# Kernel tuning notes

Measured on AMD Instinct MI355X. Metric: run time of the kernel, lower is better.

Reference implementation:

```python
import jax, jax.numpy as jnp
import numpy as np

OUTPUT_DIM = 4096
INPUT_DIM = 2048
BATCH = 8192
SPARSITY = 0.02
BOOST_STRENGTH = 100.0
TOP_K = int(np.ceil(SPARSITY * OUTPUT_DIM))  # 82


def setup_inputs() -> dict:
    key = jax.random.key(0)
    k1, k2, k3, k4 = jax.random.split(key, 4)
    # Binary input activity pattern, as expected by an HTM spatial pooler.
    x = (jax.random.uniform(k1, (BATCH, INPUT_DIM)) < 0.3).astype(jnp.float32)
    # connection = round(uniform permanence) * bernoulli(pool_density=0.9) mask -> binary.
    perm = jnp.round(jax.random.uniform(k2, (INPUT_DIM, OUTPUT_DIM)))
    mask = (jax.random.uniform(k3, (INPUT_DIM, OUTPUT_DIM)) < 0.9).astype(jnp.float32)
    connection = perm * mask
    # Average duty-cycle activations are near the target sparsity (~0.02);
    # keeping them small also keeps exp(-boost_strength * diff) in fp32 range.
    avg_activation = jax.random.uniform(k4, (1, OUTPUT_DIM)) * 0.02
    return {"x": x, "connection": connection, "avg_activation": avg_activation}


def reference(x, connection, avg_activation) -> jnp.ndarray:
    D = connection.shape[1]
    # neighbor_activity = avg_activation @ (1 - I) / (D - 1)
    # == (sum(avg) - avg) / (D - 1), avoiding the dense [D, D] matmul.
    total = jnp.sum(avg_activation, axis=1, keepdims=True)  # [1, 1]
    neighbor_activity = (total - avg_activation) / (D - 1)  # [1, D]
    boost_factor = jnp.exp(-BOOST_STRENGTH * (avg_activation - neighbor_activity))
    overlap = jnp.matmul(x, connection) * boost_factor  # [B, D]
    _, act_idx = jax.lax.top_k(overlap, TOP_K)  # [B, TOP_K]
    batch_ids = jnp.arange(x.shape[0])[:, None]  # [B, 1]
    # Scatter 1.0 into a dense one-hot activation map.
    output = jnp.zeros_like(overlap).at[batch_ids, act_idx].set(1.0)
    return output
```

## Files before the change

### kernel.cpp

```cpp
#include <hip/hip_runtime.h>
#include <math.h>

#define M_DIM 8192
#define K_DIM 2048
#define N_DIM 4096
#define TOPK  82

typedef short short8 __attribute__((ext_vector_type(8)));
typedef float f32x4 __attribute__((ext_vector_type(4)));
typedef int   i32x4 __attribute__((ext_vector_type(4)));
typedef unsigned short ushort_t;
typedef unsigned long long u64;

__device__ __forceinline__ unsigned short f2bf(float f){
  unsigned u = __float_as_uint(f);
  unsigned r = (u + 0x7FFFu + ((u >> 16) & 1u)) >> 16;
  return (unsigned short)r;
}

__device__ __forceinline__ void gload16(const void* g, void* l){
  __builtin_amdgcn_global_load_lds(
      (const __attribute__((address_space(1))) unsigned int*)g,
      (__attribute__((address_space(3))) unsigned int*)l,
      16, 0, 0);
}

__global__ __launch_bounds__(256) void prep_kernel(const float* __restrict__ X,
                                                   const float* __restrict__ Cn,
                                                   const float* __restrict__ avg,
                                                   unsigned char* __restrict__ A8,
                                                   unsigned char* __restrict__ B8,
                                                   double* __restrict__ boost){
  int bid = blockIdx.x;
  int tid = threadIdx.x;
  if (bid < 4096){
    size_t base = ((size_t)bid * 256 + tid) * 16;
    unsigned r[4];
    #pragma unroll
    for (int q = 0; q < 4; ++q){
      float4 f = *(const float4*)&X[base + q*4];
      r[q] = (unsigned)(f.x != 0.f) | ((unsigned)(f.y != 0.f) << 8)
           | ((unsigned)(f.z != 0.f) << 16) | ((unsigned)(f.w != 0.f) << 24);
    }
    uint4 o; o.x = r[0]; o.y = r[1]; o.z = r[2]; o.w = r[3];
    *(uint4*)&A8[base] = o;
  } else if (bid < 4608){
    __shared__ float s[128*132];
    int b = bid - 4096;
    int bk = b & 15, bn = b >> 4;
    int rr = tid >> 5, cc = (tid & 31)*4;
    #pragma unroll
    for (int p = 0; p < 16; ++p){
      int r = p*8 + rr;
      float4 f = *(const float4*)&Cn[((size_t)(bk*128 + r))*N_DIM + bn*128 + cc];
      *(float4*)&s[r*132 + cc] = f;
    }
    __syncthreads();
    int nn = tid >> 3, k0 = (tid & 7)*16;
    #pragma unroll
    for (int p = 0; p < 4; ++p){
      int n = p*32 + nn;
      unsigned bout[4];
      #pragma unroll
      for (int h = 0; h < 4; ++h){
        unsigned bb = 0;
        #pragma unroll
        for (int j = 0; j < 4; ++j){
          unsigned bits = __float_as_uint(s[(k0 + h*4 + j)*132 + n]);
          bb |= ((bits >> 23) & 1u) << (8*j);
        }
        bout[h] = bb;
      }
      uint4 o; o.x = bout[0]; o.y = bout[1]; o.z = bout[2]; o.w = bout[3];
      *(uint4*)&B8[((size_t)(bn*128 + n))*K_DIM + bk*128 + k0] = o;
    }
  } else {
    __shared__ double sp[4];
    __shared__ double stot;
    int lane = tid & 63, w = tid >> 6;
    double s = 0.0;
    for (int i = 0; i < 16; ++i) s += (double)avg[tid + 256*i];
    for (int off = 32; off > 0; off >>= 1) s += __shfl_down(s, off, 64);
    if (lane == 0) sp[w] = s;
    __syncthreads();
    if (tid == 0) stot = sp[0] + sp[1] + sp[2] + sp[3];
    __syncthreads();
    double tot = stot;
    for (int i = 0; i < 16; ++i){
      int j = tid + 256*i;
      double a = (double)avg[j];
      double nb = (tot - a) / 4095.0;
      boost[j] = exp(-100.0 * (a - nb));
    }
  }
}

template<typename OUT_T>
__global__ __launch_bounds__(512, 2) void gemm5_kernel(const unsigned char* __restrict__ A8,
                                                       const unsigned char* __restrict__ B8,
                                                       OUT_T* __restrict__ out){
  __shared__ unsigned char smem[65536];
  int tid = threadIdx.x;
  int lane = tid & 63, w = tid >> 6;
  unsigned bid = blockIdx.x;
  unsigned sw = (bid & 7u)*64u + (bid >> 3);
  int bn = sw & 15, bm = sw >> 4;
  int brow = bm*256, bcol = bn*256;
  int wr = w >> 2, wc = w & 3;
  int fr = lane & 15, fq = lane >> 4;
  int pl = lane >> 3;
  int sx = (lane & 7) ^ (pl & 7);
  int sp2 = sx >> 2;
  int sc = sx & 3;

  i32x4 acc[8][4];
  #pragma unroll
  for (int m = 0; m < 8; ++m)
    #pragma unroll
    for (int n = 0; n < 4; ++n) acc[m][n] = (i32x4){0,0,0,0};

  auto stage = [&](int c, int kt){
    unsigned char* Ad = smem + c*16384;
    unsigned char* Bd = smem + 32768 + c*16384;
    int kbase = kt*64;
    #pragma unroll
    for (int i = 0; i < 2; ++i){
      int R0 = w*32 + i*16;
      int r  = R0 + 2*pl + sp2;
      gload16(A8 + ((size_t)(brow + r))*K_DIM + kbase + sc*16, Ad + R0*64);
      gload16(B8 + ((size_t)(bcol + r))*K_DIM + kbase + sc*16, Bd + R0*64);
    }
  };

  auto lds_off = [&](int r)->int{
    int pair = r >> 1;
    int s = (((r & 1) << 2) + fq) ^ (pair & 7);
    return pair*128 + s*16;
  };

  stage(0, 0);
  __syncthreads();
  int cur = 0;
  for (int t = 0; t < 32; ++t){
    if (t < 31) stage(cur ^ 1, t + 1);
    const unsigned char* Ah = smem + cur*16384;
    const unsigned char* Bh = smem + 32768 + cur*16384;
    i32x4 a[8], b[4];
    #pragma unroll
    for (int n = 0; n < 4; ++n)
      b[n] = *(const i32x4*)&Bh[lds_off(wc*64 + n*16 + fr)];
    #pragma unroll
    for (int m = 0; m < 8; ++m)
      a[m] = *(const i32x4*)&Ah[lds_off(wr*128 + m*16 + fr)];
    #pragma unroll
    for (int m = 0; m < 8; ++m)
      #pragma unroll
      for (int n = 0; n < 4; ++n)
        acc[m][n] = __builtin_amdgcn_mfma_i32_16x16x64_i8(a[m], b[n], acc[m][n], 0, 0, 0);
    __syncthreads();
    cur ^= 1;
  }

  if constexpr (sizeof(OUT_T) == 2){
    unsigned short* Ct = (unsigned short*)smem;
    #pragma unroll
    for (int p = 0; p < 2; ++p){
      if (wr == p){
        #pragma unroll
        for (int m = 0; m < 8; ++m)
          #pragma unroll
          for (int n = 0; n < 4; ++n){
            int lr = m*16 + fq*4;
            int lc = wc*64 + n*16 + fr;
            #pragma unroll
            for (int j = 0; j < 4; ++j)
              Ct[(lr + j)*256 + lc] = (unsigned short)acc[m][n][j];
          }
      }
      __syncthreads();
      #pragma unroll
      for (int q = 0; q < 8; ++q){
        int idx = q*8192 + tid*16;
        int lr = idx >> 9;
        int lcb = idx & 511;
        char* gp = (char*)(out + ((size_t)(brow + p*128 + lr))*N_DIM + bcol) + lcb;
        *(uint4*)gp = *(const uint4*)&smem[idx];
      }
      __syncthreads();
    }
  } else {
    #pragma unroll
    for (int m = 0; m < 8; ++m)
      #pragma unroll
      for (int n = 0; n < 4; ++n){
        int row = brow + wr*128 + m*16 + fq*4;
        int col = bcol + wc*64 + n*16 + fr;
        #pragma unroll
        for (int j = 0; j < 4; ++j)
          out[((size_t)(row + j))*N_DIM + col] = (OUT_T)acc[m][n][j];
      }
  }
}

__global__ __launch_bounds__(256) void gemm_fb_kernel(const float* __restrict__ X,
                                                      const float* __restrict__ Cn,
                                                      float* __restrict__ out){
  __shared__ ushort_t As[128*32];
  __shared__ ushort_t Bs[128*32];
  int tid = threadIdx.x;
  int bn = blockIdx.x & 31, bm = blockIdx.x >> 5;
  int brow = bm * 128, bcol = bn * 128;
  int lane = tid & 63, w = tid >> 6;
  int wr = w >> 1, wc = w & 1;
  int fr = lane & 15, fq = lane >> 4;
  f32x4 acc[4][4];
  for (int m = 0; m < 4; ++m)
    for (int n = 0; n < 4; ++n)
      acc[m][n] = (f32x4){0.f, 0.f, 0.f, 0.f};
  int r2 = tid >> 1, h = tid & 1;
  int kr = tid >> 3, seg = tid & 7;
  for (int kk = 0; kk < K_DIM; kk += 32){
    __syncthreads();
    const float* ga = X + ((size_t)(brow + r2))*K_DIM + kk + h*16;
    unsigned pk[8];
    for (int q = 0; q < 4; ++q){
      float4 f = *(const float4*)(ga + q*4);
      pk[q*2]   = (unsigned)f2bf(f.x) | ((unsigned)f2bf(f.y) << 16);
      pk[q*2+1] = (unsigned)f2bf(f.z) | ((unsigned)f2bf(f.w) << 16);
    }
    uint4 u0; u0.x = pk[0]; u0.y = pk[1]; u0.z = pk[2]; u0.w = pk[3];
    uint4 u1; u1.x = pk[4]; u1.y = pk[5]; u1.z = pk[6]; u1.w = pk[7];
    *(uint4*)&As[r2*32 + h*16]     = u0;
    *(uint4*)&As[r2*32 + h*16 + 8] = u1;
    const float* gb = Cn + ((size_t)(kk + kr))*N_DIM + bcol + seg*16;
    for (int q = 0; q < 4; ++q){
      float4 f = *(const float4*)(gb + q*4);
      Bs[(seg*16 + q*4 + 0)*32 + kr] = f2bf(f.x);
      Bs[(seg*16 + q*4 + 1)*32 + kr] = f2bf(f.y);
      Bs[(seg*16 + q*4 + 2)*32 + kr] = f2bf(f.z);
      Bs[(seg*16 + q*4 + 3)*32 + kr] = f2bf(f.w);
    }
    __syncthreads();
    short8 a[4], b[4];
    for (int m = 0; m < 4; ++m) a[m] = *(const short8*)&As[(wr*64 + m*16 + fr)*32 + fq*8];
    for (int n = 0; n < 4; ++n) b[n] = *(const short8*)&Bs[(wc*64 + n*16 + fr)*32 + fq*8];
    for (int m = 0; m < 4; ++m)
      for (int n = 0; n < 4; ++n)
        acc[m][n] = __builtin_amdgcn_mfma_f32_16x16x32_bf16(a[m], b[n], acc[m][n], 0, 0, 0);
  }
  for (int m = 0; m < 4; ++m)
    for (int n = 0; n < 4; ++n){
      int row = brow + wr*64 + m*16 + fq*4;
      int col = bcol + wc*64 + n*16 + fr;
      for (int j = 0; j < 4; ++j)
        out[((size_t)(row + j))*N_DIM + col] = acc[m][n][j];
    }
}

#define PIDX(x) ((x) + ((x) >> 5))
#define HSZ 4224

__device__ __forceinline__ void find_bin(const unsigned* hist, unsigned* wtot,
                                         int* pB, int* pK, int tid, int Kt){
  int lane = tid & 63, w = tid >> 6;
  unsigned s = 0;
  #pragma unroll
  for (int b = 0; b < 16; ++b) s += hist[PIDX(tid*16 + b)];
  unsigned S = s;
  #pragma unroll
  for (int off = 1; off < 64; off <<= 1){
    unsigned T = __shfl_down(S, off, 64);
    if (lane + off < 64) S += T;
  }
  if (lane == 0) wtot[w] = S;
  __syncthreads();
  unsigned above = 0;
  for (int w2 = w + 1; w2 < 4; ++w2) above += wtot[w2];
  unsigned St = S + above;
  unsigned Sn = St - s;
  if (St >= (unsigned)Kt && Sn < (unsigned)Kt){
    unsigned cum = Sn;
    for (int b = 15; b >= 0; --b){
      unsigned hb = hist[PIDX(tid*16 + b)];
      cum += hb;
      if (cum >= (unsigned)Kt){ *pB = tid*16 + b; *pK = Kt - (int)(cum - hb); break; }
    }
  }
  __syncthreads();
}

template<typename CT>
__global__ __launch_bounds__(256) void topk_kernel(const CT* __restrict__ cnt,
                                                   float* __restrict__ outp,
                                                   const double* __restrict__ boost){
  __shared__ unsigned hist[HSZ];
  __shared__ unsigned wtot[4];
  __shared__ double smaxd[4];
  __shared__ int sB, sK, scnt, sTi;
  __shared__ u64 sTv;
  __shared__ u64 cbits[256];
  __shared__ int cidx[256];
  int tid = threadIdx.x;
  int lane = tid & 63, w = tid >> 6;
  const CT* rp = cnt + (size_t)blockIdx.x * N_DIM;
  float* wp = outp + (size_t)blockIdx.x * N_DIM;

  double v[16];
  #pragma unroll
  for (int g = 0; g < 4; ++g){
    int c0 = g*1024 + tid*4;
    double4 bf = *(const double4*)&boost[c0];
    if constexpr (sizeof(CT) == 2){
      ushort4 f = *(const ushort4*)&rp[c0];
      v[g*4+0] = (double)f.x * bf.x;
      v[g*4+1] = (double)f.y * bf.y;
      v[g*4+2] = (double)f.z * bf.z;
      v[g*4+3] = (double)f.w * bf.w;
    } else {
      float4 f = *(const float4*)&rp[c0];
      v[g*4+0] = (double)f.x * bf.x;
      v[g*4+1] = (double)f.y * bf.y;
      v[g*4+2] = (double)f.z * bf.z;
      v[g*4+3] = (double)f.w * bf.w;
    }
  }

  double mx = v[0];
  #pragma unroll
  for (int e = 1; e < 16; ++e) mx = fmax(mx, v[e]);
  #pragma unroll
  for (int off = 32; off > 0; off >>= 1) mx = fmax(mx, __shfl_down(mx, off, 64));
  if (lane == 0) smaxd[w] = mx;
  #pragma unroll
  for (int i = 0; i < 17; ++i){
    int x = tid + 256*i;
    if (x < HSZ) hist[x] = 0u;
  }
  if (tid == 0) scnt = 0;
  __syncthreads();

  double M = fmax(fmax(smaxd[0], smaxd[1]), fmax(smaxd[2], smaxd[3]));
  float sF = (M > 0.0) ? (float)(4095.0 / M) : 0.0f;
  unsigned bin[16];
  #pragma unroll
  for (int e = 0; e < 16; ++e)
    bin[e] = (unsigned)fminf(4095.0f, (float)v[e] * sF);
  #pragma unroll
  for (int e = 0; e < 16; ++e) atomicAdd(&hist[PIDX(bin[e])], 1u);
  __syncthreads();

  find_bin(hist, wtot, &sB, &sK, tid, TOPK);
  int B = sB, k1 = sK;

  #pragma unroll
  for (int e = 0; e < 16; ++e){
    if (bin[e] == (unsigned)B){
      int pos = atomicAdd(&scnt, 1);
      if (pos < 256){
        int g = e >> 2, j = e & 3;
        cbits[pos] = (u64)__double_as_longlong(v[e]);
        cidx[pos] = g*1024 + tid*4 + j;
      }
    }
  }
  __syncthreads();
  int Csz = scnt; if (Csz > 256) Csz = 256;
  for (int i = tid; i < Csz; i += 256){
    u64 bi = cbits[i]; int xi = cidx[i];
    int rk = 0;
    for (int j2 = 0; j2 < Csz; ++j2){
      u64 bj = cbits[j2];
      rk += (int)((bj > bi) || (bj == bi && cidx[j2] < xi));
    }
    if (rk == k1 - 1){ sTv = bi; sTi = xi; }
  }
  __syncthreads();
  double Tv = __longlong_as_double((long long)sTv);
  int Ti = sTi;
  #pragma unroll
  for (int g = 0; g < 4; ++g){
    int c0 = g*1024 + tid*4;
    float4 o;
    o.x = (v[g*4+0] > Tv || (v[g*4+0] == Tv && (c0+0) <= Ti)) ? 1.0f : 0.0f;
    o.y = (v[g*4+1] > Tv || (v[g*4+1] == Tv && (c0+1) <= Ti)) ? 1.0f : 0.0f;
    o.z = (v[g*4+2] > Tv || (v[g*4+2] == Tv && (c0+2) <= Ti)) ? 1.0f : 0.0f;
    o.w = (v[g*4+3] > Tv || (v[g*4+3] == Tv && (c0+3) <= Ti)) ? 1.0f : 0.0f;
    *(float4*)&wp[c0] = o;
  }
}

extern "C" void kernel_launch(void* const* d_in, const int* in_sizes, int n_in,
                              void* d_out, int out_size, void* d_ws, size_t ws_size,
                              hipStream_t stream){
  (void)in_sizes; (void)n_in; (void)out_size;
  const float* X   = (const float*)d_in[0];
  const float* Cn  = (const float*)d_in[1];
  const float* avg = (const float*)d_in[2];
  float* out = (float*)d_out;
  char* ws = (char*)d_ws;

  double* boost = (double*)ws;
  const size_t offA = 65536;
  unsigned char* A8 = (unsigned char*)(ws + offA);
  unsigned char* B8 = (unsigned char*)(ws + offA + (size_t)16777216);
  unsigned short* CNT = (unsigned short*)(ws + offA + (size_t)25165824);
  const size_t need_mid  = offA + (size_t)25165824;
  const size_t need_full = need_mid + (size_t)67108864;

  if (ws_size >= need_full){
    prep_kernel<<<dim3(4609), dim3(256), 0, stream>>>(X, Cn, avg, A8, B8, boost);
    gemm5_kernel<unsigned short><<<dim3(512), dim3(512), 0, stream>>>(A8, B8, CNT);
    topk_kernel<unsigned short><<<dim3(8192), dim3(256), 0, stream>>>(CNT, out, boost);
  } else if (ws_size >= need_mid){
    prep_kernel<<<dim3(4609), dim3(256), 0, stream>>>(X, Cn, avg, A8, B8, boost);
    gemm5_kernel<float><<<dim3(512), dim3(512), 0, stream>>>(A8, B8, out);
    topk_kernel<float><<<dim3(8192), dim3(256), 0, stream>>>(out, out, boost);
  } else {
    prep_kernel<<<dim3(4609), dim3(256), 0, stream>>>(X, Cn, avg, A8, B8, boost);
    gemm_fb_kernel<<<dim3(2048), dim3(256), 0, stream>>>(X, Cn, out);
    topk_kernel<float><<<dim3(8192), dim3(256), 0, stream>>>(out, out, boost);
  }
}
```

Measured before the change: 133.9 us.

## Switch binary GEMM from int8 MFMA to FP4 scaled MFMA

Binary activations and connections are packed as FP4 (value 1.0 encoded as 0x2) instead of int8, halving the bytes of the packed operands, and the GEMM uses the MI355X f8f6f4 scaled MFMA with 128-wide K per instruction. This cuts the K loop from 32 to 16 iterations and halves the global-to-LDS traffic per tile. Each operand is zero-padded from 4 to 8 dwords in registers, and accumulation moves to fp32, so counts are rounded back to integers. Exactness relies on fp32 holding small integer sums exactly.

```diff
diff --git a/kernel.cpp b/kernel.cpp
--- a/kernel.cpp
+++ b/kernel.cpp
@@ -9,6 +9,7 @@
 typedef short short8 __attribute__((ext_vector_type(8)));
 typedef float f32x4 __attribute__((ext_vector_type(4)));
 typedef int   i32x4 __attribute__((ext_vector_type(4)));
+typedef int   i32x8 __attribute__((ext_vector_type(8)));
 typedef unsigned short ushort_t;
 typedef unsigned long long u64;
 
@@ -25,28 +26,33 @@
       16, 0, 0);
 }
 
+__device__ __forceinline__ f32x4 mfma_fp4(i32x4 a, i32x4 b, f32x4 c){
+  i32x8 A; A[0]=a[0]; A[1]=a[1]; A[2]=a[2]; A[3]=a[3]; A[4]=0; A[5]=0; A[6]=0; A[7]=0;
+  i32x8 B; B[0]=b[0]; B[1]=b[1]; B[2]=b[2]; B[3]=b[3]; B[4]=0; B[5]=0; B[6]=0; B[7]=0;
+  return __builtin_amdgcn_mfma_scale_f32_16x16x128_f8f6f4(
+      A, B, c, 4, 4, 0, 0x7F7F7F7F, 0, 0x7F7F7F7F);
+}
+
 __global__ __launch_bounds__(256) void prep_kernel(const float* __restrict__ X,
                                                    const float* __restrict__ Cn,
                                                    const float* __restrict__ avg,
-                                                   unsigned char* __restrict__ A8,
-                                                   unsigned char* __restrict__ B8,
+                                                   unsigned* __restrict__ A4,
+                                                   unsigned char* __restrict__ B4,
                                                    double* __restrict__ boost){
   int bid = blockIdx.x;
   int tid = threadIdx.x;
-  if (bid < 4096){
-    size_t base = ((size_t)bid * 256 + tid) * 16;
-    unsigned r[4];
-    #pragma unroll
-    for (int q = 0; q < 4; ++q){
-      float4 f = *(const float4*)&X[base + q*4];
-      r[q] = (unsigned)(f.x != 0.f) | ((unsigned)(f.y != 0.f) << 8)
-           | ((unsigned)(f.z != 0.f) << 16) | ((unsigned)(f.w != 0.f) << 24);
-    }
-    uint4 o; o.x = r[0]; o.y = r[1]; o.z = r[2]; o.w = r[3];
-    *(uint4*)&A8[base] = o;
-  } else if (bid < 4608){
+  if (bid < 8192){
+    size_t e0 = ((size_t)bid*256 + tid)*8;
+    float4 f0 = *(const float4*)&X[e0];
+    float4 f1 = *(const float4*)&X[e0 + 4];
+    unsigned dw = (f0.x!=0.f?2u:0u)        | ((f0.y!=0.f?2u:0u)<<4)
+                | ((f0.z!=0.f?2u:0u)<<8)   | ((f0.w!=0.f?2u:0u)<<12)
+                | ((f1.x!=0.f?2u:0u)<<16)  | ((f1.y!=0.f?2u:0u)<<20)
+                | ((f1.z!=0.f?2u:0u)<<24)  | ((f1.w!=0.f?2u:0u)<<28);
+    A4[(size_t)bid*256 + tid] = dw;
+  } else if (bid < 8704){
     __shared__ float s[128*132];
-    int b = bid - 4096;
+    int b = bid - 8192;
     int bk = b & 15, bn = b >> 4;
     int rr = tid >> 5, cc = (tid & 31)*4;
     #pragma unroll
@@ -56,24 +62,23 @@
       *(float4*)&s[r*132 + cc] = f;
     }
     __syncthreads();
-    int nn = tid >> 3, k0 = (tid & 7)*16;
-    #pragma unroll
-    for (int p = 0; p < 4; ++p){
-      int n = p*32 + nn;
-      unsigned bout[4];
+    int nn = tid >> 1, kh = tid & 1;
+    unsigned dws[8];
+    #pragma unroll
+    for (int d = 0; d < 8; ++d){
+      unsigned v = 0;
       #pragma unroll
-      for (int h = 0; h < 4; ++h){
-        unsigned bb = 0;
-        #pragma unroll
-        for (int j = 0; j < 4; ++j){
-          unsigned bits = __float_as_uint(s[(k0 + h*4 + j)*132 + n]);
-          bb |= ((bits >> 23) & 1u) << (8*j);
-        }
-        bout[h] = bb;
+      for (int i = 0; i < 8; ++i){
+        int k = kh*64 + d*8 + i;
+        v |= (s[k*132 + nn] != 0.f ? 2u : 0u) << (4*i);
       }
-      uint4 o; o.x = bout[0]; o.y = bout[1]; o.z = bout[2]; o.w = bout[3];
-      *(uint4*)&B8[((size_t)(bn*128 + n))*K_DIM + bk*128 + k0] = o;
-    }
+      dws[d] = v;
+    }
+    uint4 o0; o0.x=dws[0]; o0.y=dws[1]; o0.z=dws[2]; o0.w=dws[3];
+    uint4 o1; o1.x=dws[4]; o1.y=dws[5]; o1.z=dws[6]; o1.w=dws[7];
+    size_t rowb = (size_t)(bn*128 + nn)*1024 + bk*64 + kh*32;
+    *(uint4*)&B4[rowb]      = o0;
+    *(uint4*)&B4[rowb + 16] = o1;
   } else {
     __shared__ double sp[4];
     __shared__ double stot;
@@ -96,9 +101,9 @@
 }
 
 template<typename OUT_T>
-__global__ __launch_bounds__(512, 2) void gemm5_kernel(const unsigned char* __restrict__ A8,
-                                                       const unsigned char* __restrict__ B8,
-                                                       OUT_T* __restrict__ out){
+__global__ __launch_bounds__(512, 2) void gemm5f_kernel(const unsigned char* __restrict__ A4,
+                                                        const unsigned char* __restrict__ B4,
+                                                        OUT_T* __restrict__ out){
   __shared__ unsigned char smem[65536];
   int tid = threadIdx.x;
   int lane = tid & 63, w = tid >> 6;
@@ -113,11 +118,11 @@
   int sp2 = sx >> 2;
   int sc = sx & 3;
 
-  i32x4 acc[8][4];
+  f32x4 acc[8][4];
   #pragma unroll
   for (int m = 0; m < 8; ++m)
     #pragma unroll
-    for (int n = 0; n < 4; ++n) acc[m][n] = (i32x4){0,0,0,0};
+    for (int n = 0; n < 4; ++n) acc[m][n] = (f32x4){0.f,0.f,0.f,0.f};
 
   auto stage = [&](int c, int kt){
     unsigned char* Ad = smem + c*16384;
@@ -127,8 +132,8 @@
     for (int i = 0; i < 2; ++i){
       int R0 = w*32 + i*16;
       int r  = R0 + 2*pl + sp2;
-      gload16(A8 + ((size_t)(brow + r))*K_DIM + kbase + sc*16, Ad + R0*64);
-      gload16(B8 + ((size_t)(bcol + r))*K_DIM + kbase + sc*16, Bd + R0*64);
+      gload16(A4 + ((size_t)(brow + r))*1024 + kbase + sc*16, Ad + R0*64);
+      gload16(B4 + ((size_t)(bcol + r))*1024 + kbase + sc*16, Bd + R0*64);
     }
   };
 
@@ -141,8 +146,8 @@
   stage(0, 0);
   __syncthreads();
   int cur = 0;
-  for (int t = 0; t < 32; ++t){
-    if (t < 31) stage(cur ^ 1, t + 1);
+  for (int t = 0; t < 16; ++t){
+    if (t < 15) stage(cur ^ 1, t + 1);
     const unsigned char* Ah = smem + cur*16384;
     const unsigned char* Bh = smem + 32768 + cur*16384;
     i32x4 a[8], b[4];
@@ -156,7 +161,7 @@
     for (int m = 0; m < 8; ++m)
       #pragma unroll
       for (int n = 0; n < 4; ++n)
-        acc[m][n] = __builtin_amdgcn_mfma_i32_16x16x64_i8(a[m], b[n], acc[m][n], 0, 0, 0);
+        acc[m][n] = mfma_fp4(a[m], b[n], acc[m][n]);
     __syncthreads();
     cur ^= 1;
   }
@@ -174,7 +179,7 @@
             int lc = wc*64 + n*16 + fr;
             #pragma unroll
             for (int j = 0; j < 4; ++j)
-              Ct[(lr + j)*256 + lc] = (unsigned short)acc[m][n][j];
+              Ct[(lr + j)*256 + lc] = (unsigned short)(acc[m][n][j] + 0.5f);
           }
       }
       __syncthreads();
@@ -401,22 +406,22 @@
 
   double* boost = (double*)ws;
   const size_t offA = 65536;
-  unsigned char* A8 = (unsigned char*)(ws + offA);
-  unsigned char* B8 = (unsigned char*)(ws + offA + (size_t)16777216);
+  unsigned char* A4 = (unsigned char*)(ws + offA);
+  unsigned char* B4 = (unsigned char*)(ws + offA + (size_t)8388608);
   unsigned short* CNT = (unsigned short*)(ws + offA + (size_t)25165824);
   const size_t need_mid  = offA + (size_t)25165824;
   const size_t need_full = need_mid + (size_t)67108864;
 
   if (ws_size >= need_full){
-    prep_kernel<<<dim3(4609), dim3(256), 0, stream>>>(X, Cn, avg, A8, B8, boost);
-    gemm5_kernel<unsigned short><<<dim3(512), dim3(512), 0, stream>>>(A8, B8, CNT);
+    prep_kernel<<<dim3(8705), dim3(256), 0, stream>>>(X, Cn, avg, (unsigned*)A4, B4, boost);
+    gemm5f_kernel<unsigned short><<<dim3(512), dim3(512), 0, stream>>>(A4, B4, CNT);
     topk_kernel<unsigned short><<<dim3(8192), dim3(256), 0, stream>>>(CNT, out, boost);
   } else if (ws_size >= need_mid){
-    prep_kernel<<<dim3(4609), dim3(256), 0, stream>>>(X, Cn, avg, A8, B8, boost);
-    gemm5_kernel<float><<<dim3(512), dim3(512), 0, stream>>>(A8, B8, out);
+    prep_kernel<<<dim3(8705), dim3(256), 0, stream>>>(X, Cn, avg, (unsigned*)A4, B4, boost);
+    gemm5f_kernel<float><<<dim3(512), dim3(512), 0, stream>>>(A4, B4, out);
     topk_kernel<float><<<dim3(8192), dim3(256), 0, stream>>>(out, out, boost);
   } else {
-    prep_kernel<<<dim3(4609), dim3(256), 0, stream>>>(X, Cn, avg, A8, B8, boost);
+    prep_kernel<<<dim3(8705), dim3(256), 0, stream>>>(X, Cn, avg, (unsigned*)A4, B4, boost);
     gemm_fb_kernel<<<dim3(2048), dim3(256), 0, stream>>>(X, Cn, out);
     topk_kernel<float><<<dim3(8192), dim3(256), 0, stream>>>(out, out, boost);
   }
```

New measurement: 111.0 us, median of 3. 1.21x faster.
